# Kernel optimization log

Hardware: AMD Instinct MI355X
Metric: run time of the kernel (lower is better)

## Reference

```python
import jax, jax.numpy as jnp
import numpy as np

D_MODEL = 768
D_STATE = 16
B, L = 4, 2048


def setup_inputs() -> dict:
    key = jax.random.key(0)
    ks = jax.random.split(key, 8)
    s = 1.0 / np.sqrt(D_MODEL)
    x = jax.random.normal(ks[0], (B, L, D_MODEL), jnp.float32)
    W_in = jax.random.normal(ks[1], (D_MODEL, 2 * D_MODEL), jnp.float32) * s
    b_in = jnp.zeros((2 * D_MODEL,), jnp.float32)
    W_B = jax.random.normal(ks[2], (D_MODEL, D_STATE), jnp.float32) * s
    b_B = jnp.zeros((D_STATE,), jnp.float32)
    W_C = jax.random.normal(ks[3], (D_MODEL, D_STATE), jnp.float32) * s
    b_C = jnp.zeros((D_STATE,), jnp.float32)
    W_delta = jax.random.normal(ks[4], (D_MODEL, D_MODEL), jnp.float32) * s
    b_delta = jnp.zeros((D_MODEL,), jnp.float32)
    W_out = jax.random.normal(ks[5], (D_MODEL, D_MODEL), jnp.float32) * s
    b_out = jnp.zeros((D_MODEL,), jnp.float32)
    # A_log init from the module: log(A + 1) with A[s, d] = s+1
    A_log = jnp.log(jnp.arange(1, D_STATE + 1, dtype=jnp.float32)[:, None]
                    * jnp.ones((1, D_MODEL), jnp.float32) + 1.0)
    D = jnp.ones((D_MODEL,), jnp.float32)
    return {"x": x, "W_in": W_in, "b_in": b_in, "W_B": W_B, "b_B": b_B,
            "W_C": W_C, "b_C": b_C, "W_delta": W_delta, "b_delta": b_delta,
            "W_out": W_out, "b_out": b_out, "A_log": A_log, "D": D}


def reference(x, W_in, b_in, W_B, b_B, W_C, b_C, W_delta, b_delta,
              W_out, b_out, A_log, D):
    x_proj = x @ W_in + b_in                      # (B, L, 2*d_model)
    x_main, x_gate = jnp.split(x_proj, 2, axis=-1)
    x_main = jax.nn.silu(x_main)
    B_mat = x_main @ W_B + b_B                    # (B, L, d_state)
    C_mat = x_main @ W_C + b_C                    # (B, L, d_state)
    delta = jax.nn.softplus(x_main @ W_delta + b_delta) + 0.0001
    delta = jnp.clip(delta, 0.0001, 1.0)          # (B, L, d_model)
    A = jnp.clip(-jnp.exp(A_log), -5.0, -0.1)     # (d_state, d_model)
    deltaA = jnp.exp(jnp.clip(delta[:, :, None, :] * A[None, None, :, :], -2.0, 0.0))
    deltaA = jnp.clip(deltaA, 0.05, 1.0)          # (B, L, d_state, d_model)
    deltaB_u = jnp.clip(delta[:, :, None, :] * B_mat[:, :, :, None] * x_main[:, :, None, :],
                        -5.0, 5.0)                # (B, L, d_state, d_model)

    def binary_operator(elem1, elem2):
        A1, Bu1 = elem1
        A2, Bu2 = elem2
        A_c = jnp.clip(A2 * A1, 1e-06, 10.0)
        Bu_c = jnp.clip(A2 * Bu1 + Bu2, -100.0, 100.0)
        return (A_c, Bu_c)

    # elementwise combine => scanning along axis=1 of the batched arrays is
    # identical to vmapping a per-batch scan over axis 0
    _, h_Bu = jax.lax.associative_scan(binary_operator, (deltaA, deltaB_u), axis=1)
    y = jnp.einsum('blsd,bls->bld', h_Bu, C_mat)
    y = jnp.clip(y, -10.0, 10.0)
    y = y + x_main * D[None, None, :]
    y = y * jax.nn.silu(x_gate)
    y = jnp.clip(y @ W_out + b_out, -10.0, 10.0)
    return y
```

## Files before the change

### kernel.cpp

```cpp
#include <hip/hip_runtime.h>
#include <hip/hip_bf16.h>
#include <cstdint>
#include <cstddef>

#define D_MODEL 768
#define D_STATE 16
#define BB      4
#define LL      2048
#define M_TOT   (BB*LL)
#define NCHUNK  64
#define LCH     (LL/NCHUNK)
#define N_DBC   896
#define KC      768
#define NTK     (KC/32)

typedef __attribute__((ext_vector_type(8))) short bf16x8;
typedef __attribute__((ext_vector_type(4))) float f32x4;

__device__ __forceinline__ float clampf_(float x, float lo, float hi) {
    return fminf(fmaxf(x, lo), hi);
}
__device__ __forceinline__ float siluf_(float x) {
    return x / (1.f + __expf(-x));
}
__device__ __forceinline__ unsigned short f2bf(float f) {
    unsigned u = __float_as_uint(f);
    u += 0x7fffu + ((u >> 16) & 1u);
    return (unsigned short)(u >> 16);
}
__device__ __forceinline__ float bf2f(unsigned short u) {
    return __uint_as_float(((unsigned)u) << 16);
}


__global__ __launch_bounds__(256) void k_convert_x(const float* __restrict__ x,
                                                   unsigned short* __restrict__ xb, int n4) {
    int i = blockIdx.x * 256 + threadIdx.x;
    if (i >= n4) return;
    float4 v = ((const float4*)x)[i];
    ushort4 o;
    o.x = f2bf(v.x); o.y = f2bf(v.y); o.z = f2bf(v.z); o.w = f2bf(v.w);
    ((ushort4*)xb)[i] = o;
}

__global__ __launch_bounds__(256) void k_prep_A(const float* __restrict__ A_log,
                                                float* __restrict__ A_cl, int n) {
    int i = blockIdx.x * 256 + threadIdx.x;
    if (i < n) A_cl[i] = clampf_(-__expf(A_log[i]), -5.f, -0.1f);
}

__global__ __launch_bounds__(256) void k_transpose_bf16(const float* __restrict__ src,
                                                        unsigned short* __restrict__ dst,
                                                        int R, int C) {
    __shared__ float tile[32][33];
    int tx = threadIdx.x & 31, ty = threadIdx.x >> 5;
    int c0 = blockIdx.x * 32, r0 = blockIdx.y * 32;
    #pragma unroll
    for (int rr = ty; rr < 32; rr += 8)
        tile[rr][tx] = src[(size_t)(r0 + rr) * C + c0 + tx];
    __syncthreads();
    #pragma unroll
    for (int rr = ty; rr < 32; rr += 8)
        dst[(size_t)(c0 + rr) * R + r0 + tx] = f2bf(tile[tx][rr]);
}

__global__ __launch_bounds__(256) void k_fill_bc(const float* __restrict__ W_B,
                                                 const float* __restrict__ W_C,
                                                 unsigned short* __restrict__ WdBC) {
    int idx = blockIdx.x * 256 + threadIdx.x;
    if (idx >= 128 * D_MODEL) return;
    int r = idx / D_MODEL + D_MODEL, k = idx % D_MODEL;
    unsigned short v = 0;
    if (r < D_MODEL + 16)       v = f2bf(W_B[k * 16 + (r - D_MODEL)]);
    else if (r < D_MODEL + 32)  v = f2bf(W_C[k * 16 + (r - D_MODEL - 16)]);
    WdBC[(size_t)r * D_MODEL + k] = v;
}

__global__ __launch_bounds__(256) void k_bias_dbc(const float* __restrict__ b_delta,
                                                  const float* __restrict__ b_B,
                                                  const float* __restrict__ b_C,
                                                  float* __restrict__ bias) {
    int i = blockIdx.x * 256 + threadIdx.x;
    if (i >= N_DBC) return;
    float v = 0.f;
    if (i < D_MODEL)            v = b_delta[i];
    else if (i < D_MODEL + 16)  v = b_B[i - D_MODEL];
    else if (i < D_MODEL + 32)  v = b_C[i - D_MODEL - 16];
    bias[i] = v;
}

template<int EPI>
__global__ __launch_bounds__(512) void k_gemm(const unsigned short* __restrict__ A,
                                              const unsigned short* __restrict__ Bt,
                                              const float* __restrict__ bias,
                                              int gx,
                                              float* __restrict__ out_f,
                                              float* __restrict__ out_f2,
                                              unsigned short* __restrict__ out_b0,
                                              unsigned short* __restrict__ out_b1) {
    __shared__ __align__(16) unsigned short As0[256 * 32], As1[256 * 32];
    __shared__ __align__(16) unsigned short Bs0[128 * 32], Bs1[128 * 32];
    const int tid = threadIdx.x;
    const int wave = tid >> 6, lane = tid & 63;
    const int wm = wave >> 1, wn = wave & 1;

    const int nwg = gridDim.x;
    const int wg = blockIdx.x;
    int swz = wg;
    if ((nwg & 7) == 0) {
        const int q = nwg >> 3;
        swz = (wg & 7) * q + (wg >> 3);
    }
    const int bx = swz % gx, by = swz / gx;
    const int m0 = by * 256, n0 = bx * 128;
    const int lr = lane & 15;

    const int row0 = tid >> 2, jl = tid & 3;
    const int jj = jl ^ ((row0 >> 1) & 3);
    const unsigned short* gA0 = &A [(size_t)(m0 +       row0) * KC + jl * 8];
    const unsigned short* gA1 = &A [(size_t)(m0 + 128 + row0) * KC + jl * 8];
    const unsigned short* gB0 = &Bt[(size_t)(n0 +       row0) * KC + jl * 8];
    const int wA0 = (row0 * 4 + jj) * 8;
    const int wA1 = ((row0 + 128) * 4 + jj) * 8;
    const int wB0 = (row0 * 4 + jj) * 8;

    const int swzk = (((lane >> 4) ^ (lane >> 1)) & 3) * 8;

    f32x4 acc[4][4] = {};
    float4 ra0, ra1, rb0;

    auto loadT = [&](int kt) {
        ra0 = *(const float4*)(gA0 + kt);
        ra1 = *(const float4*)(gA1 + kt);
        rb0 = *(const float4*)(gB0 + kt);
    };
    auto writeT = [&](unsigned short* Ab, unsigned short* Bb) {
        *(float4*)&Ab[wA0] = ra0;
        *(float4*)&Ab[wA1] = ra1;
        *(float4*)&Bb[wB0] = rb0;
    };
    auto computeT = [&](const unsigned short* Ab, const unsigned short* Bb) {
        bf16x8 af[4], bfr[4];
        #pragma unroll
        for (int mt = 0; mt < 4; ++mt)
            af[mt] = *(const bf16x8*)&Ab[(wm * 64 + mt * 16 + lr) * 32 + swzk];
        #pragma unroll
        for (int nt = 0; nt < 4; ++nt)
            bfr[nt] = *(const bf16x8*)&Bb[(wn * 64 + nt * 16 + lr) * 32 + swzk];
        #pragma unroll
        for (int mt = 0; mt < 4; ++mt)
            #pragma unroll
            for (int nt = 0; nt < 4; ++nt)
                acc[mt][nt] = __builtin_amdgcn_mfma_f32_16x16x32_bf16(
                    af[mt], bfr[nt], acc[mt][nt], 0, 0, 0);
    };

    loadT(0);
    writeT(As0, Bs0);
    loadT(32);
    writeT(As1, Bs1);
    asm volatile("s_waitcnt lgkmcnt(0)" ::: "memory");
    __builtin_amdgcn_sched_barrier(0);
    __builtin_amdgcn_s_barrier();
    __builtin_amdgcn_sched_barrier(0);

#define SUBSTEP(Ab, Bb, t) do {                                   \
        if ((t) + 2 < NTK) loadT(((t) + 2) << 5);                 \
        computeT(Ab, Bb);                                         \
        asm volatile("s_waitcnt lgkmcnt(0)" ::: "memory");        \
        __builtin_amdgcn_sched_barrier(0);                        \
        __builtin_amdgcn_s_barrier();                             \
        __builtin_amdgcn_sched_barrier(0);                        \
        if ((t) + 2 < NTK) writeT(Ab, Bb);                        \
    } while (0)

    for (int t = 0; t < NTK; t += 2) {
        SUBSTEP(As0, Bs0, t);
        SUBSTEP(As1, Bs1, t + 1);
    }
#undef SUBSTEP

    #pragma unroll
    for (int mt = 0; mt < 4; ++mt) {
        int row = m0 + wm * 64 + mt * 16 + (lane >> 4) * 4;
        #pragma unroll
        for (int nt = 0; nt < 4; ++nt) {
            int col = n0 + wn * 64 + nt * 16 + (lane & 15);
            #pragma unroll
            for (int i = 0; i < 4; ++i) {
                int r = row + i;
                float v = acc[mt][nt][i] + bias[col];
                if (EPI == 0) {
                    float s = siluf_(v);
                    if (col < D_MODEL) out_b0[(size_t)r * D_MODEL + col] = f2bf(s);
                    else               out_b1[(size_t)r * D_MODEL + (col - D_MODEL)] = f2bf(s);
                } else if (EPI == 1) {
                    if (col < D_MODEL) {
                        float sp = (v > 20.f) ? v : log1pf(__expf(v));
                        out_b0[(size_t)r * D_MODEL + col] = f2bf(clampf_(sp + 1e-4f, 1e-4f, 1.f));
                    } else if (col < D_MODEL + 16) {
                        out_f[(size_t)r * D_STATE + (col - D_MODEL)] = v;
                    } else if (col < D_MODEL + 32) {
                        out_f2[(size_t)r * D_STATE + (col - D_MODEL - 16)] = v;
                    }
                } else {
                    out_f[(size_t)r * D_MODEL + col] = clampf_(v, -10.f, 10.f);
                }
            }
        }
    }
}

__global__ __launch_bounds__(256) void k_scanA(const unsigned short* __restrict__ dlt,
                                               const unsigned short* __restrict__ xm,
                                               const float* __restrict__ Bm,
                                               const float* __restrict__ A_cl,
                                               float* __restrict__ h_end,
                                               float* __restrict__ Aprod) {
    const int d = blockIdx.x * 256 + threadIdx.x;
    const int c = blockIdx.y, b = blockIdx.z;
    __shared__ float Bsh[LCH][D_STATE];
    const int rowbase = b * LL + c * LCH;
    for (int i = threadIdx.x; i < LCH * D_STATE; i += 256)
        ((float*)Bsh)[i] = Bm[(size_t)rowbase * D_STATE + i];
    __syncthreads();

    float Asv[16], h[16], ap[16];
    #pragma unroll
    for (int s = 0; s < 16; ++s) {
        Asv[s] = A_cl[s * D_MODEL + d];
        h[s] = 0.f; ap[s] = 1.f;
    }
    for (int tt = 0; tt < LCH; ++tt) {
        const size_t rowoff = (size_t)(rowbase + tt);
        float dltv = bf2f(dlt[rowoff * D_MODEL + d]);
        float xv   = bf2f(xm [rowoff * D_MODEL + d]);
        float dx = dltv * xv;
        #pragma unroll
        for (int s = 0; s < 16; ++s) {
            float dA  = __expf(fmaxf(dltv * Asv[s], -2.f));
            float dBu = clampf_(dx * Bsh[tt][s], -5.f, 5.f);
            h[s] = clampf_(fmaf(dA, h[s], dBu), -100.f, 100.f);
            ap[s] *= dA;
        }
    }
    const size_t off = (((size_t)b * NCHUNK + c) * D_STATE) * D_MODEL + d;
    #pragma unroll
    for (int s = 0; s < 16; ++s) {
        h_end[off + (size_t)s * D_MODEL] = h[s];
        Aprod[off + (size_t)s * D_MODEL] = ap[s];
    }
}

__global__ __launch_bounds__(256) void k_scanB(const float* __restrict__ h_end,
                                               const float* __restrict__ Aprod,
                                               float* __restrict__ h_in) {
    const int idx = blockIdx.x * 256 + threadIdx.x;
    const int d = idx % D_MODEL;
    const int rest = idx / D_MODEL;
    const int s = rest & 15, b = rest >> 4;
    float hc = 0.f;
    for (int c = 0; c < NCHUNK; ++c) {
        const size_t off = (((size_t)b * NCHUNK + c) * D_STATE + s) * D_MODEL + d;
        h_in[off] = hc;
        hc = Aprod[off] * hc + h_end[off];
    }
}

__global__ __launch_bounds__(256) void k_scanC(const unsigned short* __restrict__ dlt,
                                               const unsigned short* __restrict__ xm,
                                               const float* __restrict__ Bm,
                                               const float* __restrict__ Cm,
                                               const float* __restrict__ A_cl,
                                               const float* __restrict__ h_in,
                                               const float* __restrict__ Dvec,
                                               const unsigned short* __restrict__ gate,
                                               unsigned short* __restrict__ ymid) {
    const int d = blockIdx.x * 256 + threadIdx.x;
    const int c = blockIdx.y, b = blockIdx.z;
    __shared__ float Bsh[LCH][D_STATE];
    __shared__ float Csh[LCH][D_STATE];
    const int rowbase = b * LL + c * LCH;
    for (int i = threadIdx.x; i < LCH * D_STATE; i += 256) {
        ((float*)Bsh)[i] = Bm[(size_t)rowbase * D_STATE + i];
        ((float*)Csh)[i] = Cm[(size_t)rowbase * D_STATE + i];
    }
    __syncthreads();

    float Asv[16], h[16];
    const size_t coff = (((size_t)b * NCHUNK + c) * D_STATE) * D_MODEL + d;
    #pragma unroll
    for (int s = 0; s < 16; ++s) {
        Asv[s] = A_cl[s * D_MODEL + d];
        h[s] = h_in[coff + (size_t)s * D_MODEL];
    }
    const float Dv = Dvec[d];
    for (int tt = 0; tt < LCH; ++tt) {
        const size_t rowoff = (size_t)(rowbase + tt);
        float dltv = bf2f(dlt[rowoff * D_MODEL + d]);
        float xv   = bf2f(xm [rowoff * D_MODEL + d]);
        float dx = dltv * xv;
        float y = 0.f;
        #pragma unroll
        for (int s = 0; s < 16; ++s) {
            float dA  = __expf(fmaxf(dltv * Asv[s], -2.f));
            float dBu = clampf_(dx * Bsh[tt][s], -5.f, 5.f);
            h[s] = clampf_(fmaf(dA, h[s], dBu), -100.f, 100.f);
            y = fmaf(h[s], Csh[tt][s], y);
        }
        y = clampf_(y, -10.f, 10.f);
        y = fmaf(xv, Dv, y);
        y *= bf2f(gate[rowoff * D_MODEL + d]);
        ymid[rowoff * D_MODEL + d] = f2bf(y);
    }
}

extern "C" void kernel_launch(void* const* d_in, const int* in_sizes, int n_in,
                              void* d_out, int out_size, void* d_ws, size_t ws_size,
                              hipStream_t stream) {
    const float* x       = (const float*)d_in[0];
    const float* W_in    = (const float*)d_in[1];
    const float* b_in    = (const float*)d_in[2];
    const float* W_B     = (const float*)d_in[3];
    const float* b_B     = (const float*)d_in[4];
    const float* W_C     = (const float*)d_in[5];
    const float* b_C     = (const float*)d_in[6];
    const float* W_delta = (const float*)d_in[7];
    const float* b_delta = (const float*)d_in[8];
    const float* W_out   = (const float*)d_in[9];
    const float* b_out   = (const float*)d_in[10];
    const float* A_log   = (const float*)d_in[11];
    const float* Dvec    = (const float*)d_in[12];
    float* out = (float*)d_out;

    char* p = (char*)d_ws;
    auto alloc = [&](size_t bytes) {
        char* r = p;
        p += (bytes + 255) & ~(size_t)255;
        return r;
    };
    unsigned short* xb    = (unsigned short*)alloc((size_t)M_TOT * D_MODEL * 2);
    unsigned short* Wint  = (unsigned short*)alloc((size_t)2 * D_MODEL * D_MODEL * 2);
    unsigned short* WdBC  = (unsigned short*)alloc((size_t)N_DBC * D_MODEL * 2);
    unsigned short* Wot   = (unsigned short*)alloc((size_t)D_MODEL * D_MODEL * 2);
    float*          bdbc  = (float*)alloc((size_t)N_DBC * 4);
    unsigned short* xm_b  = (unsigned short*)alloc((size_t)M_TOT * D_MODEL * 2);
    unsigned short* gate_b= (unsigned short*)alloc((size_t)M_TOT * D_MODEL * 2);
    unsigned short* dlt_b = (unsigned short*)alloc((size_t)M_TOT * D_MODEL * 2);
    float*          Bm    = (float*)alloc((size_t)M_TOT * D_STATE * 4);
    float*          Cm    = (float*)alloc((size_t)M_TOT * D_STATE * 4);
    float*          A_cl  = (float*)alloc((size_t)D_STATE * D_MODEL * 4);
    float*          h_end = (float*)alloc((size_t)BB * NCHUNK * D_STATE * D_MODEL * 4);
    float*          Aprod = (float*)alloc((size_t)BB * NCHUNK * D_STATE * D_MODEL * 4);
    float*          h_in  = (float*)alloc((size_t)BB * NCHUNK * D_STATE * D_MODEL * 4);
    unsigned short* ymid  = (unsigned short*)alloc((size_t)M_TOT * D_MODEL * 2);

    k_convert_x<<<(M_TOT * D_MODEL / 4 + 255) / 256, 256, 0, stream>>>(x, xb, M_TOT * D_MODEL / 4);
    k_prep_A<<<(D_STATE * D_MODEL + 255) / 256, 256, 0, stream>>>(A_log, A_cl, D_STATE * D_MODEL);
    k_transpose_bf16<<<dim3(2 * D_MODEL / 32, D_MODEL / 32), 256, 0, stream>>>(W_in, Wint, D_MODEL, 2 * D_MODEL);
    k_transpose_bf16<<<dim3(D_MODEL / 32, D_MODEL / 32), 256, 0, stream>>>(W_delta, WdBC, D_MODEL, D_MODEL);
    k_fill_bc<<<(128 * D_MODEL + 255) / 256, 256, 0, stream>>>(W_B, W_C, WdBC);
    k_bias_dbc<<<(N_DBC + 255) / 256, 256, 0, stream>>>(b_delta, b_B, b_C, bdbc);
    k_transpose_bf16<<<dim3(D_MODEL / 32, D_MODEL / 32), 256, 0, stream>>>(W_out, Wot, D_MODEL, D_MODEL);

    k_gemm<0><<<dim3((2 * D_MODEL / 128) * (M_TOT / 256)), 512, 0, stream>>>(
        xb, Wint, b_in, 2 * D_MODEL / 128, nullptr, nullptr, xm_b, gate_b);
    k_gemm<1><<<dim3((N_DBC / 128) * (M_TOT / 256)), 512, 0, stream>>>(
        xm_b, WdBC, bdbc, N_DBC / 128, Bm, Cm, dlt_b, nullptr);
    k_scanA<<<dim3(D_MODEL / 256, NCHUNK, BB), 256, 0, stream>>>(dlt_b, xm_b, Bm, A_cl, h_end, Aprod);
    k_scanB<<<(BB * D_STATE * D_MODEL) / 256, 256, 0, stream>>>(h_end, Aprod, h_in);
    k_scanC<<<dim3(D_MODEL / 256, NCHUNK, BB), 256, 0, stream>>>(
        dlt_b, xm_b, Bm, Cm, A_cl, h_in, Dvec, gate_b, ymid);
    k_gemm<2><<<dim3((D_MODEL / 128) * (M_TOT / 256)), 512, 0, stream>>>(
        ymid, Wot, b_out, D_MODEL / 128, out, nullptr, nullptr, nullptr);
}
```

Baseline: 203.1 us.

## Halve GEMM workgroup to 4 waves, load B fragments directly from global

The GEMM kernel now runs 256 threads per block instead of 512, and each wave computes a 128x64 output sub-tile (8x4 MFMA tiles). B operand fragments are no longer staged through LDS. Each wave reads them from global memory straight into registers, double-buffered one k-step ahead. This cuts LDS traffic and footprint and doubles A-fragment reuse per wave. In exchange it raises register pressure (32 accumulators) and relies on the cache to serve redundant B reads across waves with wm differing.

```diff
diff --git a/kernel.cpp b/kernel.cpp
--- a/kernel.cpp
+++ b/kernel.cpp
@@ -90,7 +90,7 @@
 }
 
 template<int EPI>
-__global__ __launch_bounds__(512) void k_gemm(const unsigned short* __restrict__ A,
+__global__ __launch_bounds__(256) void k_gemm(const unsigned short* __restrict__ A,
                                               const unsigned short* __restrict__ Bt,
                                               const float* __restrict__ bias,
                                               int gx,
@@ -99,7 +99,6 @@
                                               unsigned short* __restrict__ out_b0,
                                               unsigned short* __restrict__ out_b1) {
     __shared__ __align__(16) unsigned short As0[256 * 32], As1[256 * 32];
-    __shared__ __align__(16) unsigned short Bs0[128 * 32], Bs1[128 * 32];
     const int tid = threadIdx.x;
     const int wave = tid >> 6, lane = tid & 63;
     const int wm = wave >> 1, wn = wave & 1;
@@ -117,75 +116,84 @@
 
     const int row0 = tid >> 2, jl = tid & 3;
     const int jj = jl ^ ((row0 >> 1) & 3);
-    const unsigned short* gA0 = &A [(size_t)(m0 +       row0) * KC + jl * 8];
-    const unsigned short* gA1 = &A [(size_t)(m0 + 128 + row0) * KC + jl * 8];
-    const unsigned short* gB0 = &Bt[(size_t)(n0 +       row0) * KC + jl * 8];
-    const int wA0 = (row0 * 4 + jj) * 8;
-    const int wA1 = ((row0 + 128) * 4 + jj) * 8;
-    const int wB0 = (row0 * 4 + jj) * 8;
+    const unsigned short* gA0 = &A[(size_t)(m0 + row0      ) * KC + jl * 8];
+    const unsigned short* gA1 = &A[(size_t)(m0 + row0 +  64) * KC + jl * 8];
+    const unsigned short* gA2 = &A[(size_t)(m0 + row0 + 128) * KC + jl * 8];
+    const unsigned short* gA3 = &A[(size_t)(m0 + row0 + 192) * KC + jl * 8];
+    const int wA0 = ((row0      ) * 4 + jj) * 8;
+    const int wA1 = ((row0 +  64) * 4 + jj) * 8;
+    const int wA2 = ((row0 + 128) * 4 + jj) * 8;
+    const int wA3 = ((row0 + 192) * 4 + jj) * 8;
 
     const int swzk = (((lane >> 4) ^ (lane >> 1)) & 3) * 8;
 
-    f32x4 acc[4][4] = {};
-    float4 ra0, ra1, rb0;
-
-    auto loadT = [&](int kt) {
+    const unsigned short* gB = &Bt[(size_t)(n0 + wn * 64 + lr) * KC + (lane >> 4) * 8];
+
+    f32x4 acc[8][4] = {};
+    float4 ra0, ra1, ra2, ra3;
+    bf16x8 bA[4], bB[4];
+
+    auto loadA = [&](int kt) {
         ra0 = *(const float4*)(gA0 + kt);
         ra1 = *(const float4*)(gA1 + kt);
-        rb0 = *(const float4*)(gB0 + kt);
-    };
-    auto writeT = [&](unsigned short* Ab, unsigned short* Bb) {
+        ra2 = *(const float4*)(gA2 + kt);
+        ra3 = *(const float4*)(gA3 + kt);
+    };
+    auto writeA = [&](unsigned short* Ab) {
         *(float4*)&Ab[wA0] = ra0;
         *(float4*)&Ab[wA1] = ra1;
-        *(float4*)&Bb[wB0] = rb0;
-    };
-    auto computeT = [&](const unsigned short* Ab, const unsigned short* Bb) {
-        bf16x8 af[4], bfr[4];
-        #pragma unroll
-        for (int mt = 0; mt < 4; ++mt)
-            af[mt] = *(const bf16x8*)&Ab[(wm * 64 + mt * 16 + lr) * 32 + swzk];
+        *(float4*)&Ab[wA2] = ra2;
+        *(float4*)&Ab[wA3] = ra3;
+    };
+    auto loadB = [&](bf16x8* bf, int kt) {
         #pragma unroll
         for (int nt = 0; nt < 4; ++nt)
-            bfr[nt] = *(const bf16x8*)&Bb[(wn * 64 + nt * 16 + lr) * 32 + swzk];
-        #pragma unroll
-        for (int mt = 0; mt < 4; ++mt)
+            bf[nt] = *(const bf16x8*)(gB + (size_t)nt * 16 * KC + kt);
+    };
+    auto computeT = [&](const unsigned short* Ab, const bf16x8* bf) {
+        #pragma unroll
+        for (int mt = 0; mt < 8; ++mt) {
+            bf16x8 af = *(const bf16x8*)&Ab[(wm * 128 + mt * 16 + lr) * 32 + swzk];
             #pragma unroll
             for (int nt = 0; nt < 4; ++nt)
                 acc[mt][nt] = __builtin_amdgcn_mfma_f32_16x16x32_bf16(
-                    af[mt], bfr[nt], acc[mt][nt], 0, 0, 0);
-    };
-
-    loadT(0);
-    writeT(As0, Bs0);
-    loadT(32);
-    writeT(As1, Bs1);
+                    af, bf[nt], acc[mt][nt], 0, 0, 0);
+        }
+    };
+
+    loadA(0);
+    writeA(As0);
+    loadA(32);
+    writeA(As1);
+    loadB(bA, 0);
     asm volatile("s_waitcnt lgkmcnt(0)" ::: "memory");
     __builtin_amdgcn_sched_barrier(0);
     __builtin_amdgcn_s_barrier();
     __builtin_amdgcn_sched_barrier(0);
 
-#define SUBSTEP(Ab, Bb, t) do {                                   \
-        if ((t) + 2 < NTK) loadT(((t) + 2) << 5);                 \
-        computeT(Ab, Bb);                                         \
+#define SUBSTEP(Ab, t, bcur, bnext) do {                          \
+        if ((t) + 2 < NTK) loadA(((t) + 2) << 5);                 \
+        if ((t) + 1 < NTK) loadB(bnext, ((t) + 1) << 5);          \
+        computeT(Ab, bcur);                                       \
         asm volatile("s_waitcnt lgkmcnt(0)" ::: "memory");        \
         __builtin_amdgcn_sched_barrier(0);                        \
         __builtin_amdgcn_s_barrier();                             \
         __builtin_amdgcn_sched_barrier(0);                        \
-        if ((t) + 2 < NTK) writeT(Ab, Bb);                        \
+        if ((t) + 2 < NTK) writeA(Ab);                            \
     } while (0)
 
     for (int t = 0; t < NTK; t += 2) {
-        SUBSTEP(As0, Bs0, t);
-        SUBSTEP(As1, Bs1, t + 1);
+        SUBSTEP(As0, t,     bA, bB);
+        SUBSTEP(As1, t + 1, bB, bA);
     }
 #undef SUBSTEP
 
     #pragma unroll
-    for (int mt = 0; mt < 4; ++mt) {
-        int row = m0 + wm * 64 + mt * 16 + (lane >> 4) * 4;
+    for (int mt = 0; mt < 8; ++mt) {
+        int row = m0 + wm * 128 + mt * 16 + (lane >> 4) * 4;
         #pragma unroll
         for (int nt = 0; nt < 4; ++nt) {
-            int col = n0 + wn * 64 + nt * 16 + (lane & 15);
+            int col = n0 + wn * 64 + nt * 16 + lr;
             #pragma unroll
             for (int i = 0; i < 4; ++i) {
                 int r = row + i;
@@ -363,14 +371,14 @@
     k_bias_dbc<<<(N_DBC + 255) / 256, 256, 0, stream>>>(b_delta, b_B, b_C, bdbc);
     k_transpose_bf16<<<dim3(D_MODEL / 32, D_MODEL / 32), 256, 0, stream>>>(W_out, Wot, D_MODEL, D_MODEL);
 
-    k_gemm<0><<<dim3((2 * D_MODEL / 128) * (M_TOT / 256)), 512, 0, stream>>>(
+    k_gemm<0><<<dim3((2 * D_MODEL / 128) * (M_TOT / 256)), 256, 0, stream>>>(
         xb, Wint, b_in, 2 * D_MODEL / 128, nullptr, nullptr, xm_b, gate_b);
-    k_gemm<1><<<dim3((N_DBC / 128) * (M_TOT / 256)), 512, 0, stream>>>(
+    k_gemm<1><<<dim3((N_DBC / 128) * (M_TOT / 256)), 256, 0, stream>>>(
         xm_b, WdBC, bdbc, N_DBC / 128, Bm, Cm, dlt_b, nullptr);
     k_scanA<<<dim3(D_MODEL / 256, NCHUNK, BB), 256, 0, stream>>>(dlt_b, xm_b, Bm, A_cl, h_end, Aprod);
     k_scanB<<<(BB * D_STATE * D_MODEL) / 256, 256, 0, stream>>>(h_end, Aprod, h_in);
     k_scanC<<<dim3(D_MODEL / 256, NCHUNK, BB), 256, 0, stream>>>(
         dlt_b, xm_b, Bm, Cm, A_cl, h_in, Dvec, gate_b, ymid);
-    k_gemm<2><<<dim3((D_MODEL / 128) * (M_TOT / 256)), 512, 0, stream>>>(
+    k_gemm<2><<<dim3((D_MODEL / 128) * (M_TOT / 256)), 256, 0, stream>>>(
         ymid, Wot, b_out, D_MODEL / 128, out, nullptr, nullptr, nullptr);
 }
```

Measured after the change: 295.2 us. 1.45x slower.

## Retile bf16 GEMM to 128x128 blocks with BK=64 and 256 threads

Applied to the files above, without the earlier changes.

Changes the GEMM workgroup tile from 256x128 with 8 waves and BK=32 to 128x128 with 4 waves and BK=64. Shared-memory staging moves to 64-wide rows with an XOR swizzle over 8 slots, and each thread loads four 16-byte chunks per operand per stage. The goal is fewer barrier/sync steps per K, more MFMAs between barriers, and more workgroups for better CU fill. The trade-off is more global loads per thread and a different LDS footprint, which may affect occupancy.

```diff
diff --git a/kernel.cpp b/kernel.cpp
--- a/kernel.cpp
+++ b/kernel.cpp
@@ -12,7 +12,8 @@
 #define LCH     (LL/NCHUNK)
 #define N_DBC   896
 #define KC      768
-#define NTK     (KC/32)
+#define BK      64
+#define NT2     (KC/BK)
 
 typedef __attribute__((ext_vector_type(8))) short bf16x8;
 typedef __attribute__((ext_vector_type(4))) float f32x4;
@@ -90,7 +91,7 @@
 }
 
 template<int EPI>
-__global__ __launch_bounds__(512) void k_gemm(const unsigned short* __restrict__ A,
+__global__ __launch_bounds__(256) void k_gemm(const unsigned short* __restrict__ A,
                                               const unsigned short* __restrict__ Bt,
                                               const float* __restrict__ bias,
                                               int gx,
@@ -98,11 +99,12 @@
                                               float* __restrict__ out_f2,
                                               unsigned short* __restrict__ out_b0,
                                               unsigned short* __restrict__ out_b1) {
-    __shared__ __align__(16) unsigned short As0[256 * 32], As1[256 * 32];
-    __shared__ __align__(16) unsigned short Bs0[128 * 32], Bs1[128 * 32];
+    __shared__ __align__(16) unsigned short As0[128 * 64], As1[128 * 64];
+    __shared__ __align__(16) unsigned short Bs0[128 * 64], Bs1[128 * 64];
     const int tid = threadIdx.x;
     const int wave = tid >> 6, lane = tid & 63;
     const int wm = wave >> 1, wn = wave & 1;
+    const int lr = lane & 15;
 
     const int nwg = gridDim.x;
     const int wg = blockIdx.x;
@@ -112,52 +114,61 @@
         swz = (wg & 7) * q + (wg >> 3);
     }
     const int bx = swz % gx, by = swz / gx;
-    const int m0 = by * 256, n0 = bx * 128;
-    const int lr = lane & 15;
-
-    const int row0 = tid >> 2, jl = tid & 3;
-    const int jj = jl ^ ((row0 >> 1) & 3);
-    const unsigned short* gA0 = &A [(size_t)(m0 +       row0) * KC + jl * 8];
-    const unsigned short* gA1 = &A [(size_t)(m0 + 128 + row0) * KC + jl * 8];
-    const unsigned short* gB0 = &Bt[(size_t)(n0 +       row0) * KC + jl * 8];
-    const int wA0 = (row0 * 4 + jj) * 8;
-    const int wA1 = ((row0 + 128) * 4 + jj) * 8;
-    const int wB0 = (row0 * 4 + jj) * 8;
-
-    const int swzk = (((lane >> 4) ^ (lane >> 1)) & 3) * 8;
+    const int m0 = by * 128, n0 = bx * 128;
+
+    const unsigned short* gAsrc[4];
+    const unsigned short* gBsrc[4];
+    int woff[4];
+    #pragma unroll
+    for (int g = 0; g < 4; ++g) {
+        int c = g * 256 + tid;
+        int row = c >> 3, jl = c & 7;
+        int slot = jl ^ (row & 7);
+        gAsrc[g] = &A [(size_t)(m0 + row) * KC + jl * 8];
+        gBsrc[g] = &Bt[(size_t)(n0 + row) * KC + jl * 8];
+        woff[g] = row * 64 + slot * 8;
+    }
 
     f32x4 acc[4][4] = {};
-    float4 ra0, ra1, rb0;
+    float4 ra[4], rb[4];
 
     auto loadT = [&](int kt) {
-        ra0 = *(const float4*)(gA0 + kt);
-        ra1 = *(const float4*)(gA1 + kt);
-        rb0 = *(const float4*)(gB0 + kt);
+        #pragma unroll
+        for (int g = 0; g < 4; ++g) {
+            ra[g] = *(const float4*)(gAsrc[g] + kt);
+            rb[g] = *(const float4*)(gBsrc[g] + kt);
+        }
     };
     auto writeT = [&](unsigned short* Ab, unsigned short* Bb) {
-        *(float4*)&Ab[wA0] = ra0;
-        *(float4*)&Ab[wA1] = ra1;
-        *(float4*)&Bb[wB0] = rb0;
+        #pragma unroll
+        for (int g = 0; g < 4; ++g) {
+            *(float4*)&Ab[woff[g]] = ra[g];
+            *(float4*)&Bb[woff[g]] = rb[g];
+        }
     };
     auto computeT = [&](const unsigned short* Ab, const unsigned short* Bb) {
-        bf16x8 af[4], bfr[4];
-        #pragma unroll
-        for (int mt = 0; mt < 4; ++mt)
-            af[mt] = *(const bf16x8*)&Ab[(wm * 64 + mt * 16 + lr) * 32 + swzk];
-        #pragma unroll
-        for (int nt = 0; nt < 4; ++nt)
-            bfr[nt] = *(const bf16x8*)&Bb[(wn * 64 + nt * 16 + lr) * 32 + swzk];
-        #pragma unroll
-        for (int mt = 0; mt < 4; ++mt)
+        #pragma unroll
+        for (int kh = 0; kh < 2; ++kh) {
+            const int so = ((kh * 4 + (lane >> 4)) ^ (lr & 7)) * 8;
+            bf16x8 af[4], bfr[4];
+            #pragma unroll
+            for (int mt = 0; mt < 4; ++mt)
+                af[mt] = *(const bf16x8*)&Ab[(wm * 64 + mt * 16 + lr) * 64 + so];
             #pragma unroll
             for (int nt = 0; nt < 4; ++nt)
-                acc[mt][nt] = __builtin_amdgcn_mfma_f32_16x16x32_bf16(
-                    af[mt], bfr[nt], acc[mt][nt], 0, 0, 0);
+                bfr[nt] = *(const bf16x8*)&Bb[(wn * 64 + nt * 16 + lr) * 64 + so];
+            #pragma unroll
+            for (int mt = 0; mt < 4; ++mt)
+                #pragma unroll
+                for (int nt = 0; nt < 4; ++nt)
+                    acc[mt][nt] = __builtin_amdgcn_mfma_f32_16x16x32_bf16(
+                        af[mt], bfr[nt], acc[mt][nt], 0, 0, 0);
+        }
     };
 
     loadT(0);
     writeT(As0, Bs0);
-    loadT(32);
+    loadT(BK);
     writeT(As1, Bs1);
     asm volatile("s_waitcnt lgkmcnt(0)" ::: "memory");
     __builtin_amdgcn_sched_barrier(0);
@@ -165,16 +176,16 @@
     __builtin_amdgcn_sched_barrier(0);
 
 #define SUBSTEP(Ab, Bb, t) do {                                   \
-        if ((t) + 2 < NTK) loadT(((t) + 2) << 5);                 \
+        if ((t) + 2 < NT2) loadT(((t) + 2) * BK);                 \
         computeT(Ab, Bb);                                         \
         asm volatile("s_waitcnt lgkmcnt(0)" ::: "memory");        \
         __builtin_amdgcn_sched_barrier(0);                        \
         __builtin_amdgcn_s_barrier();                             \
         __builtin_amdgcn_sched_barrier(0);                        \
-        if ((t) + 2 < NTK) writeT(Ab, Bb);                        \
+        if ((t) + 2 < NT2) writeT(Ab, Bb);                        \
     } while (0)
 
-    for (int t = 0; t < NTK; t += 2) {
+    for (int t = 0; t < NT2; t += 2) {
         SUBSTEP(As0, Bs0, t);
         SUBSTEP(As1, Bs1, t + 1);
     }
@@ -185,7 +196,7 @@
         int row = m0 + wm * 64 + mt * 16 + (lane >> 4) * 4;
         #pragma unroll
         for (int nt = 0; nt < 4; ++nt) {
-            int col = n0 + wn * 64 + nt * 16 + (lane & 15);
+            int col = n0 + wn * 64 + nt * 16 + lr;
             #pragma unroll
             for (int i = 0; i < 4; ++i) {
                 int r = row + i;
@@ -363,14 +374,14 @@
     k_bias_dbc<<<(N_DBC + 255) / 256, 256, 0, stream>>>(b_delta, b_B, b_C, bdbc);
     k_transpose_bf16<<<dim3(D_MODEL / 32, D_MODEL / 32), 256, 0, stream>>>(W_out, Wot, D_MODEL, D_MODEL);
 
-    k_gemm<0><<<dim3((2 * D_MODEL / 128) * (M_TOT / 256)), 512, 0, stream>>>(
+    k_gemm<0><<<dim3((2 * D_MODEL / 128) * (M_TOT / 128)), 256, 0, stream>>>(
         xb, Wint, b_in, 2 * D_MODEL / 128, nullptr, nullptr, xm_b, gate_b);
-    k_gemm<1><<<dim3((N_DBC / 128) * (M_TOT / 256)), 512, 0, stream>>>(
+    k_gemm<1><<<dim3((N_DBC / 128) * (M_TOT / 128)), 256, 0, stream>>>(
         xm_b, WdBC, bdbc, N_DBC / 128, Bm, Cm, dlt_b, nullptr);
     k_scanA<<<dim3(D_MODEL / 256, NCHUNK, BB), 256, 0, stream>>>(dlt_b, xm_b, Bm, A_cl, h_end, Aprod);
     k_scanB<<<(BB * D_STATE * D_MODEL) / 256, 256, 0, stream>>>(h_end, Aprod, h_in);
     k_scanC<<<dim3(D_MODEL / 256, NCHUNK, BB), 256, 0, stream>>>(
         dlt_b, xm_b, Bm, Cm, A_cl, h_in, Dvec, gate_b, ymid);
-    k_gemm<2><<<dim3((D_MODEL / 128) * (M_TOT / 256)), 512, 0, stream>>>(
+    k_gemm<2><<<dim3((D_MODEL / 128) * (M_TOT / 128)), 256, 0, stream>>>(
         ymid, Wot, b_out, D_MODEL / 128, out, nullptr, nullptr, nullptr);
 }
```

Measured after the change: 300.4 us. 47.9% more time.
